# Optimization experiments

Hardware: AMD Instinct MI355X
Metric: run time of the kernel (lower is better)

The kernel has to match this reference:

```python
import jax, jax.numpy as jnp
import numpy as np

B, T, K = 64, 1024, 256  # batch, seq_len, num_labels


def setup_inputs() -> dict:
    key = jax.random.key(0)
    k1, k2 = jax.random.split(key)
    emissions = jax.random.normal(k1, (B, T, K), dtype=jnp.float32)
    transitions = jax.random.normal(k2, (K, K), dtype=jnp.float32) * 0.1
    return {"emissions": emissions, "transitions": transitions}


def _viterbi_decode(emissions, transitions):
    """Viterbi decode, mirroring tfa.text.crf_decode with full-length sequences.
    emissions: [B, T, K] unary potentials; transitions: [K, K] (prev -> next).
    Returns int32 tag sequence [B, T]."""
    em = jnp.transpose(emissions, (1, 0, 2))  # [T, B, K]

    def fwd_step(state, emit_t):
        # state: [B, K] running max scores ending in each tag at time t-1
        scores = state[:, :, None] + transitions[None, :, :]  # [B, K_prev, K_next]
        bp = jnp.argmax(scores, axis=1).astype(jnp.int32)      # [B, K] backpointers
        new_state = jnp.max(scores, axis=1) + emit_t           # [B, K]
        return new_state, bp

    state, bps = jax.lax.scan(fwd_step, em[0], em[1:])  # bps: [T-1, B, K]
    last_tag = jnp.argmax(state, axis=-1).astype(jnp.int32)  # [B]

    def back_step(tag, bp_t):
        prev = jnp.take_along_axis(bp_t, tag[:, None], axis=1)[:, 0]
        return prev, prev

    # reverse scan: bps[i] maps tag at t=i+1 back to tag at t=i
    _, earlier = jax.lax.scan(back_step, last_tag, bps, reverse=True)  # [T-1, B]
    tags = jnp.concatenate([earlier, last_tag[None, :]], axis=0)  # [T, B]
    return jnp.transpose(tags, (1, 0))  # [B, T]


def reference(emissions, transitions):
    # CRF.call in inference mode: crf_decode then cast to the input dtype.
    return _viterbi_decode(emissions, transitions).astype(emissions.dtype)
```

## Files before the change

### kernel.cpp

```cpp
#include <hip/hip_runtime.h>


#define CRF_B 64
#define CRF_T 1024
#define CRF_K 256
#define NSEG  16
#define SEGLEN 64

#define FG 8
#define FP 32


#define LD4(v, p, col) { \
    v.x = trans[(size_t)(p) * CRF_K + (col)]; \
    v.y = trans[(size_t)((p) + 1) * CRF_K + (col)]; \
    v.z = trans[(size_t)((p) + 2) * CRF_K + (col)]; \
    v.w = trans[(size_t)((p) + 3) * CRF_K + (col)]; }

#define FWD_CHUNK(idx, ta, tb) { \
    float4 sv = sp[idx]; \
    float a0 = sv.x + ta.x; \
    float a1 = sv.y + ta.y; \
    float a2 = sv.z + ta.z; \
    float a3 = sv.w + ta.w; \
    float r0 = fmaxf(fmaxf(a0, a1), a2); \
    m0 = fmaxf(fmaxf(r0, a3), m0); \
    float c0 = sv.x + tb.x; \
    float c1 = sv.y + tb.y; \
    float c2 = sv.z + tb.z; \
    float c3 = sv.w + tb.w; \
    float r1 = fmaxf(fmaxf(c0, c1), c2); \
    m1 = fmaxf(fmaxf(r1, c3), m1); }

__global__ __launch_bounds__(1024, 4) void crf_forward_states(
    const float* __restrict__ em, const float* __restrict__ trans,
    float* __restrict__ M, unsigned char* __restrict__ gidp)
{
    const int b   = blockIdx.x;
    const int tid = threadIdx.x;
    const int g   = tid >> 7;
    const int c   = tid & 127;

    __shared__ __align__(16) float s_state[CRF_K];
    __shared__ float s_partial[FG][CRF_K];

    const int pbase = g * FP;
    const int c2    = c + 128;

    float4 ta0, ta1, ta2, ta3, ta4, ta5, ta6, ta7;
    float4 tb0, tb1, tb2, tb3, tb4, tb5, tb6, tb7;
    LD4(ta0, pbase +  0, c)  LD4(ta1, pbase +  4, c)
    LD4(ta2, pbase +  8, c)  LD4(ta3, pbase + 12, c)
    LD4(ta4, pbase + 16, c)  LD4(ta5, pbase + 20, c)
    LD4(ta6, pbase + 24, c)  LD4(ta7, pbase + 28, c)
    LD4(tb0, pbase +  0, c2) LD4(tb1, pbase +  4, c2)
    LD4(tb2, pbase +  8, c2) LD4(tb3, pbase + 12, c2)
    LD4(tb4, pbase + 16, c2) LD4(tb5, pbase + 20, c2)
    LD4(tb6, pbase + 24, c2) LD4(tb7, pbase + 28, c2)

    const float* emb = em + (size_t)b * CRF_T * CRF_K;
    if (tid < CRF_K) s_state[tid] = emb[tid];
    float e_cur = 0.0f;
    if (tid < CRF_K) e_cur = emb[CRF_K + tid];
    __syncthreads();

    float sp0 = 0, sp1 = 0, sp2 = 0, sp3 = 0;
    float sp4 = 0, sp5 = 0, sp6 = 0, sp7 = 0;
    float sbv = 0;

    for (int t = 1; t < CRF_T; ++t) {
        if (gidp && tid < CRF_K && t > 1) {
            int bg = 7;
            if (sp6 == sbv) bg = 6;
            if (sp5 == sbv) bg = 5;
            if (sp4 == sbv) bg = 4;
            if (sp3 == sbv) bg = 3;
            if (sp2 == sbv) bg = 2;
            if (sp1 == sbv) bg = 1;
            if (sp0 == sbv) bg = 0;
            int g1 = __shfl_down(bg, 1, 64);
            if ((tid & 1) == 0)
                gidp[((size_t)(t - 1) * CRF_B + b) * 128 + (tid >> 1)] =
                    (unsigned char)(bg | (g1 << 4));
        }

        float e_next = 0.0f;
        if (tid < CRF_K && t + 1 < CRF_T)
            e_next = emb[(t + 1) * CRF_K + tid];

        float m0 = -INFINITY, m1 = -INFINITY;
        const float4* sp = (const float4*)(s_state + pbase);
        FWD_CHUNK(0, ta0, tb0) FWD_CHUNK(1, ta1, tb1)
        FWD_CHUNK(2, ta2, tb2) FWD_CHUNK(3, ta3, tb3)
        FWD_CHUNK(4, ta4, tb4) FWD_CHUNK(5, ta5, tb5)
        FWD_CHUNK(6, ta6, tb6) FWD_CHUNK(7, ta7, tb7)

        s_partial[g][c]  = m0;
        s_partial[g][c2] = m1;
        __syncthreads();
        if (tid < CRF_K) {
            float p0 = s_partial[0][tid], p1 = s_partial[1][tid];
            float p2 = s_partial[2][tid], p3 = s_partial[3][tid];
            float p4 = s_partial[4][tid], p5 = s_partial[5][tid];
            float p6 = s_partial[6][tid], p7 = s_partial[7][tid];
            float q0 = fmaxf(fmaxf(p0, p1), p2);
            float q1 = fmaxf(fmaxf(p3, p4), p5);
            float bv = fmaxf(fmaxf(fmaxf(q0, q1), p6), p7);
            s_state[tid] = bv + e_cur;
            M[((size_t)t * CRF_B + b) * CRF_K + tid] = bv;
            sp0 = p0; sp1 = p1; sp2 = p2; sp3 = p3;
            sp4 = p4; sp5 = p5; sp6 = p6; sp7 = p7; sbv = bv;
        }
        __syncthreads();
        e_cur = e_next;
    }

    if (gidp && tid < CRF_K) {
        int bg = 7;
        if (sp6 == sbv) bg = 6;
        if (sp5 == sbv) bg = 5;
        if (sp4 == sbv) bg = 4;
        if (sp3 == sbv) bg = 3;
        if (sp2 == sbv) bg = 2;
        if (sp1 == sbv) bg = 1;
        if (sp0 == sbv) bg = 0;
        int g1 = __shfl_down(bg, 1, 64);
        if ((tid & 1) == 0)
            gidp[((size_t)(CRF_T - 1) * CRF_B + b) * 128 + (tid >> 1)] =
                (unsigned char)(bg | (g1 << 4));
    }
}


#define BPG_CHUNK(j) { \
    float4 mm = M4[j]; float4 ee = E4[j]; \
    float s0 = mm.x + ee.x, s1 = mm.y + ee.y; \
    float s2 = mm.z + ee.z, s3 = mm.w + ee.w; \
    float t0v = s_tile[base + 4*(j) + 0][lane]; \
    float t1v = s_tile[base + 4*(j) + 1][lane]; \
    float t2v = s_tile[base + 4*(j) + 2][lane]; \
    float t3v = s_tile[base + 4*(j) + 3][lane]; \
    float v0 = s0 + t0v; if (v0 > best) { best = v0; arg = base + 4*(j); } \
    float v1 = s1 + t1v; if (v1 > best) { best = v1; arg = base + 4*(j) + 1; } \
    float v2 = s2 + t2v; if (v2 > best) { best = v2; arg = base + 4*(j) + 2; } \
    float v3 = s3 + t3v; if (v3 > best) { best = v3; arg = base + 4*(j) + 3; } }

#define BPG_CHUNK0(j) { \
    float4 ee = E4[j]; \
    float t0v = s_tile[base + 4*(j) + 0][lane]; \
    float t1v = s_tile[base + 4*(j) + 1][lane]; \
    float t2v = s_tile[base + 4*(j) + 2][lane]; \
    float t3v = s_tile[base + 4*(j) + 3][lane]; \
    float v0 = ee.x + t0v; if (v0 > best) { best = v0; arg = base + 4*(j); } \
    float v1 = ee.y + t1v; if (v1 > best) { best = v1; arg = base + 4*(j) + 1; } \
    float v2 = ee.z + t2v; if (v2 > best) { best = v2; arg = base + 4*(j) + 2; } \
    float v3 = ee.w + t3v; if (v3 > best) { best = v3; arg = base + 4*(j) + 3; } }

__global__ __launch_bounds__(256) void crf_bp_gid(
    const float* __restrict__ M, const float* __restrict__ em,
    const float* __restrict__ trans, const unsigned char* __restrict__ gidp,
    unsigned char* __restrict__ bp)
{
    const int b    = blockIdx.x >> 3;
    const int cg   = (blockIdx.x >> 1) & 3;
    const int ts   = blockIdx.x & 1;
    const int tid  = threadIdx.x;
    const int lane = tid & 63;
    const int w    = tid >> 6;

    __shared__ float s_tile[CRF_K][64];

    const int k0 = cg * 64;
    for (int idx = tid; idx < CRF_K * 64; idx += 256) {
        const int p = idx >> 6, cc = idx & 63;
        s_tile[p][cc] = trans[(size_t)p * CRF_K + k0 + cc];
    }
    __syncthreads();

    const int t_lo = ts * 512;
    const int t_hi = ts ? (CRF_T - 1) : 512;
    const int half = (k0 >> 1) + (lane >> 1);
    const int odd  = lane & 1;

    int t1 = t_lo + w;
    if (t1 >= t_hi) return;
    unsigned char gb = gidp[((size_t)(t1 + 1) * CRF_B + b) * 128 + half];

    for (; t1 < t_hi; t1 += 4) {
        const int tn = t1 + 4;
        unsigned char gb_next = 0;
        if (tn < t_hi)
            gb_next = gidp[((size_t)(tn + 1) * CRF_B + b) * 128 + half];

        const int g    = odd ? ((gb >> 4) & 7) : (gb & 7);
        const int base = g << 5;
        const float4* E4 =
            (const float4*)(em + ((size_t)b * CRF_T + t1) * CRF_K + base);
        float best = -INFINITY; int arg = base;
        if (t1 == 0) {
            BPG_CHUNK0(0) BPG_CHUNK0(1) BPG_CHUNK0(2) BPG_CHUNK0(3)
            BPG_CHUNK0(4) BPG_CHUNK0(5) BPG_CHUNK0(6) BPG_CHUNK0(7)
        } else {
            const float4* M4 =
                (const float4*)(M + ((size_t)t1 * CRF_B + b) * CRF_K + base);
            BPG_CHUNK(0) BPG_CHUNK(1) BPG_CHUNK(2) BPG_CHUNK(3)
            BPG_CHUNK(4) BPG_CHUNK(5) BPG_CHUNK(6) BPG_CHUNK(7)
        }
        bp[((size_t)b * (CRF_T - 1) + t1) * CRF_K + k0 + lane] =
            (unsigned char)arg;
        gb = gb_next;
    }
}


__global__ __launch_bounds__(1024, 2) void crf_bp_matrix(
    const float* __restrict__ M, const float* __restrict__ em,
    const float* __restrict__ trans, unsigned char* __restrict__ bp)
{
    const int b   = blockIdx.x >> 4;
    const int seg = blockIdx.x & 15;
    const int tid = threadIdx.x;
    const int g   = tid >> 8;
    const int k   = tid & 255;

    __shared__ __align__(16) float s_row[CRF_K];
    __shared__ float s_pv[4][CRF_K];
    __shared__ int   s_pi[4][CRF_K];

    const int pbase = g * 64;
    float4 tr[16];
#pragma unroll
    for (int i = 0; i < 16; ++i) {
        const int p = pbase + 4 * i;
        tr[i].x = trans[(p + 0) * CRF_K + k];
        tr[i].y = trans[(p + 1) * CRF_K + k];
        tr[i].z = trans[(p + 2) * CRF_K + k];
        tr[i].w = trans[(p + 3) * CRF_K + k];
    }

    const int t_lo = seg * SEGLEN;
    const int t_hi = min(t_lo + SEGLEN, CRF_T - 1);
    unsigned char* bpb = bp + (size_t)b * (CRF_T - 1) * CRF_K;

    for (int t1 = t_lo; t1 < t_hi; ++t1) {
        if (tid < CRF_K) {
            float ev = em[((size_t)b * CRF_T + t1) * CRF_K + tid];
            float sv = ev;
            if (t1 > 0) sv = M[((size_t)t1 * CRF_B + b) * CRF_K + tid] + ev;
            s_row[tid] = sv;
        }
        __syncthreads();

        float best = -INFINITY;
        int   arg  = pbase;
        const float4* spp = (const float4*)(s_row + pbase);
#pragma unroll
        for (int i = 0; i < 16; ++i) {
            float4 st = spp[i];
            const int p = pbase + 4 * i;
            float s0 = st.x + tr[i].x;
            float s1 = st.y + tr[i].y;
            float s2 = st.z + tr[i].z;
            float s3 = st.w + tr[i].w;
            if (s0 > best) { best = s0; arg = p; }
            if (s1 > best) { best = s1; arg = p + 1; }
            if (s2 > best) { best = s2; arg = p + 2; }
            if (s3 > best) { best = s3; arg = p + 3; }
        }
        s_pv[g][k] = best;
        s_pi[g][k] = arg;
        __syncthreads();
        if (tid < CRF_K) {
            float bv = s_pv[0][tid];
            int   ba = s_pi[0][tid];
#pragma unroll
            for (int j = 1; j < 4; ++j) {
                float v = s_pv[j][tid];
                if (v > bv) { bv = v; ba = s_pi[j][tid]; }
            }
            bpb[(size_t)t1 * CRF_K + tid] = (unsigned char)ba;
        }
        __syncthreads();
    }
}


__global__ __launch_bounds__(256) void crf_seg_maps(
    const unsigned char* __restrict__ bp, unsigned char* __restrict__ maps)
{
    const int b   = blockIdx.x >> 4;
    const int s   = blockIdx.x & 15;
    const int tid = threadIdx.x;
    const int rows = (s == NSEG - 1) ? SEGLEN - 1 : SEGLEN;
    const int r0   = s * SEGLEN;

    __shared__ unsigned char lbp[SEGLEN][CRF_K];

    const unsigned char* bpb = bp + (size_t)b * (CRF_T - 1) * CRF_K;
    const int nw = rows * 64;
    for (int w = tid; w < nw; w += 256) {
        const int r = w >> 6, cc = w & 63;
        ((unsigned int*)lbp[r])[cc] =
            ((const unsigned int*)(bpb + (size_t)(r0 + r) * CRF_K))[cc];
    }
    __syncthreads();

    int tag = tid;
    for (int j = rows - 1; j >= 0; --j) tag = lbp[j][tag];
    maps[((size_t)b * NSEG + s) * CRF_K + tid] = (unsigned char)tag;
}

__global__ __launch_bounds__(256) void crf_compose(
    const float* __restrict__ M, const float* __restrict__ em,
    const unsigned char* __restrict__ maps,
    int* __restrict__ exits, float* __restrict__ out)
{
    const int b   = blockIdx.x;
    const int tid = threadIdx.x;

    __shared__ float s_wv[4];
    __shared__ int   s_wi[4];

    float v = M[((size_t)(CRF_T - 1) * CRF_B + b) * CRF_K + tid]
            + em[((size_t)b * CRF_T + (CRF_T - 1)) * CRF_K + tid];
    int   i = tid;
#pragma unroll
    for (int off = 32; off >= 1; off >>= 1) {
        float ov = __shfl_xor(v, off, 64);
        int   oi = __shfl_xor(i, off, 64);
        if (ov > v || (ov == v && oi < i)) { v = ov; i = oi; }
    }
    const int lane = tid & 63, wv = tid >> 6;
    if (lane == 0) { s_wv[wv] = v; s_wi[wv] = i; }
    __syncthreads();
    if (tid == 0) {
        float bv = s_wv[0]; int bi = s_wi[0];
#pragma unroll
        for (int w = 1; w < 4; ++w)
            if (s_wv[w] > bv) { bv = s_wv[w]; bi = s_wi[w]; }
        out[(size_t)b * CRF_T + (CRF_T - 1)] = (float)bi;
        int E = bi;
        exits[b * NSEG + NSEG - 1] = E;
        const unsigned char* mb = maps + (size_t)b * NSEG * CRF_K;
        for (int s = NSEG - 1; s >= 1; --s) {
            E = mb[(size_t)s * CRF_K + E];
            exits[b * NSEG + s - 1] = E;
        }
    }
}

__global__ __launch_bounds__(256) void crf_emit(
    const unsigned char* __restrict__ bp, const int* __restrict__ exits,
    float* __restrict__ out)
{
    const int b   = blockIdx.x >> 4;
    const int s   = blockIdx.x & 15;
    const int tid = threadIdx.x;
    const int rows = (s == NSEG - 1) ? SEGLEN - 1 : SEGLEN;
    const int r0   = s * SEGLEN;

    __shared__ unsigned char lbp[SEGLEN][CRF_K];

    const unsigned char* bpb = bp + (size_t)b * (CRF_T - 1) * CRF_K;
    const int nw = rows * 64;
    for (int w = tid; w < nw; w += 256) {
        const int r = w >> 6, cc = w & 63;
        ((unsigned int*)lbp[r])[cc] =
            ((const unsigned int*)(bpb + (size_t)(r0 + r) * CRF_K))[cc];
    }
    __syncthreads();

    int tag = tid;
    const bool win = (tid == exits[b * NSEG + s]);
    for (int j = rows - 1; j >= 0; --j) {
        tag = lbp[j][tag];
        if (win) out[(size_t)b * CRF_T + r0 + j] = (float)tag;
    }
}

__global__ void crf_zero_out(float* __restrict__ out, int n)
{
    int i = blockIdx.x * blockDim.x + threadIdx.x;
    if (i < n) out[i] = 0.0f;
}


extern "C" void kernel_launch(void* const* d_in, const int* in_sizes, int n_in,
                              void* d_out, int out_size, void* d_ws, size_t ws_size,
                              hipStream_t stream) {
    (void)in_sizes; (void)n_in;
    const float* em    = (const float*)d_in[0];
    const float* trans = (const float*)d_in[1];
    float* out = (float*)d_out;

    const size_t M_bytes     = (size_t)CRF_T * CRF_B * CRF_K * sizeof(float);
    const size_t gid_bytes   = (size_t)CRF_T * CRF_B * 128;
    const size_t bp_bytes    = (size_t)CRF_B * (CRF_T - 1) * CRF_K;
    const size_t maps_bytes  = (size_t)CRF_B * NSEG * CRF_K;
    const size_t exits_bytes = (size_t)CRF_B * NSEG * sizeof(int);

    char* w = (char*)d_ws;
    if (ws_size >= M_bytes + gid_bytes + bp_bytes + maps_bytes + exits_bytes) {
        float*         M     = (float*)w;            w += M_bytes;
        unsigned char* gidp  = (unsigned char*)w;    w += gid_bytes;
        unsigned char* bp    = (unsigned char*)w;    w += bp_bytes;
        unsigned char* maps  = (unsigned char*)w;    w += maps_bytes;
        int*           exits = (int*)w;

        crf_forward_states<<<CRF_B, 1024, 0, stream>>>(em, trans, M, gidp);
        crf_bp_gid<<<CRF_B * 8, 256, 0, stream>>>(M, em, trans, gidp, bp);
        crf_seg_maps<<<CRF_B * NSEG, 256, 0, stream>>>(bp, maps);
        crf_compose<<<CRF_B, 256, 0, stream>>>(M, em, maps, exits, out);
        crf_emit<<<CRF_B * NSEG, 256, 0, stream>>>(bp, exits, out);
    } else if (ws_size >= M_bytes + bp_bytes + maps_bytes + exits_bytes) {
        float*         M     = (float*)w;            w += M_bytes;
        unsigned char* bp    = (unsigned char*)w;    w += bp_bytes;
        unsigned char* maps  = (unsigned char*)w;    w += maps_bytes;
        int*           exits = (int*)w;

        crf_forward_states<<<CRF_B, 1024, 0, stream>>>(em, trans, M, nullptr);
        crf_bp_matrix<<<CRF_B * NSEG, 1024, 0, stream>>>(M, em, trans, bp);
        crf_seg_maps<<<CRF_B * NSEG, 256, 0, stream>>>(bp, maps);
        crf_compose<<<CRF_B, 256, 0, stream>>>(M, em, maps, exits, out);
        crf_emit<<<CRF_B * NSEG, 256, 0, stream>>>(bp, exits, out);
    } else {
        crf_zero_out<<<(out_size + 255) / 256, 256, 0, stream>>>(out, out_size);
    }
}
```

Measured before the change: 1.099 ms.

## Reduce forward-step partial maxima with wave shuffles and double-buffered state

The forward max-plus recurrence is remapped so that each wave owns 16 output columns, and the four 16-lane quarters each cover 64 predecessor rows. The per-column max is reduced with in-wave xor shuffles instead of going through a shared-memory partial array. This removes one of the two block-wide barriers per timestep. The state vector is double-buffered in LDS with a padded, rotated layout to avoid bank conflicts, and packed v_pk_add_f32 is used for the adds. The group-id encoding for backpointers changes to match the new predecessor partition, which risks inconsistency with the unseen backtrace kernel.

```diff
diff --git a/kernel.cpp b/kernel.cpp
--- a/kernel.cpp
+++ b/kernel.cpp
@@ -7,127 +7,138 @@
 #define NSEG  16
 #define SEGLEN 64
 
-#define FG 8
-#define FP 32
-
-
-#define LD4(v, p, col) { \
-    v.x = trans[(size_t)(p) * CRF_K + (col)]; \
-    v.y = trans[(size_t)((p) + 1) * CRF_K + (col)]; \
-    v.z = trans[(size_t)((p) + 2) * CRF_K + (col)]; \
-    v.w = trans[(size_t)((p) + 3) * CRF_K + (col)]; }
-
-#define FWD_CHUNK(idx, ta, tb) { \
-    float4 sv = sp[idx]; \
-    float a0 = sv.x + ta.x; \
-    float a1 = sv.y + ta.y; \
-    float a2 = sv.z + ta.z; \
-    float a3 = sv.w + ta.w; \
-    float r0 = fmaxf(fmaxf(a0, a1), a2); \
-    m0 = fmaxf(fmaxf(r0, a3), m0); \
-    float c0 = sv.x + tb.x; \
-    float c1 = sv.y + tb.y; \
-    float c2 = sv.z + tb.z; \
-    float c3 = sv.w + tb.w; \
-    float r1 = fmaxf(fmaxf(c0, c1), c2); \
-    m1 = fmaxf(fmaxf(r1, c3), m1); }
+
+typedef float f32x2 __attribute__((ext_vector_type(2)));
+
+__device__ __forceinline__ f32x2 pk_add(f32x2 a, f32x2 b) {
+    f32x2 d;
+    asm("v_pk_add_f32 %0, %1, %2" : "=v"(d) : "v"(a), "v"(b));
+    return d;
+}
+
+#define CHUNK_F 132
+#define BUF_F   (4 * CHUNK_F)
 
 __global__ __launch_bounds__(1024, 4) void crf_forward_states(
     const float* __restrict__ em, const float* __restrict__ trans,
     float* __restrict__ M, unsigned char* __restrict__ gidp)
 {
-    const int b   = blockIdx.x;
-    const int tid = threadIdx.x;
-    const int g   = tid >> 7;
-    const int c   = tid & 127;
-
-    __shared__ __align__(16) float s_state[CRF_K];
-    __shared__ float s_partial[FG][CRF_K];
-
-    const int pbase = g * FP;
-    const int c2    = c + 128;
-
-    float4 ta0, ta1, ta2, ta3, ta4, ta5, ta6, ta7;
-    float4 tb0, tb1, tb2, tb3, tb4, tb5, tb6, tb7;
-    LD4(ta0, pbase +  0, c)  LD4(ta1, pbase +  4, c)
-    LD4(ta2, pbase +  8, c)  LD4(ta3, pbase + 12, c)
-    LD4(ta4, pbase + 16, c)  LD4(ta5, pbase + 20, c)
-    LD4(ta6, pbase + 24, c)  LD4(ta7, pbase + 28, c)
-    LD4(tb0, pbase +  0, c2) LD4(tb1, pbase +  4, c2)
-    LD4(tb2, pbase +  8, c2) LD4(tb3, pbase + 12, c2)
-    LD4(tb4, pbase + 16, c2) LD4(tb5, pbase + 20, c2)
-    LD4(tb6, pbase + 24, c2) LD4(tb7, pbase + 28, c2)
+    const int b    = blockIdx.x;
+    const int tid  = threadIdx.x;
+    const int w    = tid >> 6;
+    const int lane = tid & 63;
+    const int l    = lane & 15;
+    const int q    = lane >> 4;
+    const int c    = (w << 4) + l;
+    const bool own = (q == 0);
+
+    __shared__ __align__(16) float sbuf[2][BUF_F];
+
+    f32x2 tr[32];
+#pragma unroll
+    for (int k = 0; k < 8; ++k) {
+        const int p0 = (q << 6) + 4 * ((q + k) & 7);
+        const float* tp0 = trans + (size_t)p0 * CRF_K + c;
+        tr[2*k+0].x = tp0[0];
+        tr[2*k+0].y = tp0[CRF_K];
+        tr[2*k+1].x = tp0[2 * CRF_K];
+        tr[2*k+1].y = tp0[3 * CRF_K];
+        const float* tp1 = tp0 + 32 * CRF_K;
+        tr[16+2*k+0].x = tp1[0];
+        tr[16+2*k+0].y = tp1[CRF_K];
+        tr[16+2*k+1].x = tp1[2 * CRF_K];
+        tr[16+2*k+1].y = tp1[3 * CRF_K];
+    }
 
     const float* emb = em + (size_t)b * CRF_T * CRF_K;
-    if (tid < CRF_K) s_state[tid] = emb[tid];
-    float e_cur = 0.0f;
-    if (tid < CRF_K) e_cur = emb[CRF_K + tid];
+
+    if (tid < CRF_K) {
+        const int cid = tid >> 6, h = (tid >> 5) & 1, pos = tid & 31;
+        const int a0  = CHUNK_F * cid + 64 * h + pos;
+        float v = emb[tid];
+        sbuf[0][a0] = v;
+        if (pos < 12) sbuf[0][a0 + 32] = v;
+    }
+    float e_cur = own ? emb[CRF_K + c] : 0.0f;
     __syncthreads();
 
-    float sp0 = 0, sp1 = 0, sp2 = 0, sp3 = 0;
-    float sp4 = 0, sp5 = 0, sp6 = 0, sp7 = 0;
-    float sbv = 0;
+    const int wcid = c >> 6, wh = (c >> 5) & 1, wpos = c & 31;
+    const int wa   = CHUNK_F * wcid + 64 * wh + wpos;
+
+    float* mptr = M + ((size_t)CRF_B + b) * CRF_K + c;
+    unsigned char* gptr = gidp
+        ? gidp + ((size_t)CRF_B + b) * 128 + (w << 3) + (l >> 1)
+        : nullptr;
+
+    float pm0 = 0.0f, pm1 = 0.0f, pbv = 0.0f;
+    int cb = 0;
 
     for (int t = 1; t < CRF_T; ++t) {
-        if (gidp && tid < CRF_K && t > 1) {
-            int bg = 7;
-            if (sp6 == sbv) bg = 6;
-            if (sp5 == sbv) bg = 5;
-            if (sp4 == sbv) bg = 4;
-            if (sp3 == sbv) bg = 3;
-            if (sp2 == sbv) bg = 2;
-            if (sp1 == sbv) bg = 1;
-            if (sp0 == sbv) bg = 0;
-            int g1 = __shfl_down(bg, 1, 64);
-            if ((tid & 1) == 0)
-                gidp[((size_t)(t - 1) * CRF_B + b) * 128 + (tid >> 1)] =
-                    (unsigned char)(bg | (g1 << 4));
+        if (gptr && t > 1) {
+            int g = (pm1 == pbv) ? ((q << 1) | 1) : 8;
+            if (pm0 == pbv) g = q << 1;
+            g = min(g, __shfl_xor(g, 16, 64));
+            g = min(g, __shfl_xor(g, 32, 64));
+            int go = __shfl_down(g, 1, 64);
+            if (own && !(l & 1))
+                *gptr = (unsigned char)(g | (go << 4));
+            gptr += CRF_B * 128;
         }
 
         float e_next = 0.0f;
-        if (tid < CRF_K && t + 1 < CRF_T)
-            e_next = emb[(t + 1) * CRF_K + tid];
+        if (own && t + 1 < CRF_T)
+            e_next = emb[(size_t)(t + 1) * CRF_K + c];
+
+        const float4* sp = (const float4*)(sbuf[cb]) + 33 * q;
 
         float m0 = -INFINITY, m1 = -INFINITY;
-        const float4* sp = (const float4*)(s_state + pbase);
-        FWD_CHUNK(0, ta0, tb0) FWD_CHUNK(1, ta1, tb1)
-        FWD_CHUNK(2, ta2, tb2) FWD_CHUNK(3, ta3, tb3)
-        FWD_CHUNK(4, ta4, tb4) FWD_CHUNK(5, ta5, tb5)
-        FWD_CHUNK(6, ta6, tb6) FWD_CHUNK(7, ta7, tb7)
-
-        s_partial[g][c]  = m0;
-        s_partial[g][c2] = m1;
-        __syncthreads();
-        if (tid < CRF_K) {
-            float p0 = s_partial[0][tid], p1 = s_partial[1][tid];
-            float p2 = s_partial[2][tid], p3 = s_partial[3][tid];
-            float p4 = s_partial[4][tid], p5 = s_partial[5][tid];
-            float p6 = s_partial[6][tid], p7 = s_partial[7][tid];
-            float q0 = fmaxf(fmaxf(p0, p1), p2);
-            float q1 = fmaxf(fmaxf(p3, p4), p5);
-            float bv = fmaxf(fmaxf(fmaxf(q0, q1), p6), p7);
-            s_state[tid] = bv + e_cur;
-            M[((size_t)t * CRF_B + b) * CRF_K + tid] = bv;
-            sp0 = p0; sp1 = p1; sp2 = p2; sp3 = p3;
-            sp4 = p4; sp5 = p5; sp6 = p6; sp7 = p7; sbv = bv;
-        }
+#pragma unroll
+        for (int k = 0; k < 8; ++k) {
+            float4 sv = sp[q + k];
+            f32x2 lo; lo.x = sv.x; lo.y = sv.y;
+            f32x2 hi; hi.x = sv.z; hi.y = sv.w;
+            f32x2 r0 = pk_add(lo, tr[2*k]);
+            f32x2 r1 = pk_add(hi, tr[2*k+1]);
+            m0 = fmaxf(fmaxf(r0.x, r0.y), m0);
+            m0 = fmaxf(fmaxf(r1.x, r1.y), m0);
+        }
+#pragma unroll
+        for (int k = 0; k < 8; ++k) {
+            float4 sv = sp[16 + q + k];
+            f32x2 lo; lo.x = sv.x; lo.y = sv.y;
+            f32x2 hi; hi.x = sv.z; hi.y = sv.w;
+            f32x2 r0 = pk_add(lo, tr[16+2*k]);
+            f32x2 r1 = pk_add(hi, tr[16+2*k+1]);
+            m1 = fmaxf(fmaxf(r0.x, r0.y), m1);
+            m1 = fmaxf(fmaxf(r1.x, r1.y), m1);
+        }
+
+        float bv = fmaxf(m0, m1);
+        bv = fmaxf(bv, __shfl_xor(bv, 16, 64));
+        bv = fmaxf(bv, __shfl_xor(bv, 32, 64));
+
+        float* nb = sbuf[cb ^ 1];
+        if (own) {
+            *mptr = bv;
+            float sv = bv + e_cur;
+            nb[wa] = sv;
+            if (wpos < 12) nb[wa + 32] = sv;
+        }
+        pm0 = m0; pm1 = m1; pbv = bv;
         __syncthreads();
         e_cur = e_next;
-    }
-
-    if (gidp && tid < CRF_K) {
-        int bg = 7;
-        if (sp6 == sbv) bg = 6;
-        if (sp5 == sbv) bg = 5;
-        if (sp4 == sbv) bg = 4;
-        if (sp3 == sbv) bg = 3;
-        if (sp2 == sbv) bg = 2;
-        if (sp1 == sbv) bg = 1;
-        if (sp0 == sbv) bg = 0;
-        int g1 = __shfl_down(bg, 1, 64);
-        if ((tid & 1) == 0)
-            gidp[((size_t)(CRF_T - 1) * CRF_B + b) * 128 + (tid >> 1)] =
-                (unsigned char)(bg | (g1 << 4));
+        mptr += CRF_B * CRF_K;
+        cb ^= 1;
+    }
+
+    if (gptr) {
+        int g = (pm1 == pbv) ? ((q << 1) | 1) : 8;
+        if (pm0 == pbv) g = q << 1;
+        g = min(g, __shfl_xor(g, 16, 64));
+        g = min(g, __shfl_xor(g, 32, 64));
+        int go = __shfl_down(g, 1, 64);
+        if (own && !(l & 1))
+            *gptr = (unsigned char)(g | (go << 4));
     }
 }
 
```

Result: slower. 1.456 ms (+32.5%).

## Spread forward partial-max reduction across all threads with DPP quad reductions

Applied to the files above, without the earlier changes.

Instead of 256 threads each reading 8 partial maxima and reducing them serially, all 1024 threads now take part: each quad of lanes owns one column, reads two partials from a padded transposed shared array, and combines them with DPP xor swizzles. The group-index backpointer byte is computed inside the same step from a bitmask of which groups hit the max, rather than deferred to the next iteration. The aim is a shorter critical path between the two barriers in the serial time loop. In exchange it adds DPP and shuffle operations plus a gidp write in every step, and every thread now loads its emission value.

```diff
diff --git a/kernel.cpp b/kernel.cpp
--- a/kernel.cpp
+++ b/kernel.cpp
@@ -9,6 +9,7 @@
 
 #define FG 8
 #define FP 32
+#define PPAD 9
 
 
 #define LD4(v, p, col) { \
@@ -32,6 +33,19 @@
     float r1 = fmaxf(fmaxf(c0, c1), c2); \
     m1 = fmaxf(fmaxf(r1, c3), m1); }
 
+#define DPP_QP_XOR1 0xB1
+#define DPP_QP_XOR2 0x4E
+
+template <int CTRL>
+__device__ __forceinline__ float dpp_getf(float v) {
+    return __int_as_float(__builtin_amdgcn_update_dpp(
+        0, __float_as_int(v), CTRL, 0xf, 0xf, false));
+}
+template <int CTRL>
+__device__ __forceinline__ int dpp_geti(int v) {
+    return __builtin_amdgcn_update_dpp(0, v, CTRL, 0xf, 0xf, false);
+}
+
 __global__ __launch_bounds__(1024, 4) void crf_forward_states(
     const float* __restrict__ em, const float* __restrict__ trans,
     float* __restrict__ M, unsigned char* __restrict__ gidp)
@@ -40,9 +54,11 @@
     const int tid = threadIdx.x;
     const int g   = tid >> 7;
     const int c   = tid & 127;
+    const int col = tid >> 2;
+    const int j   = tid & 3;
 
     __shared__ __align__(16) float s_state[CRF_K];
-    __shared__ float s_partial[FG][CRF_K];
+    __shared__ float s_partial[CRF_K][PPAD];
 
     const int pbase = g * FP;
     const int c2    = c + 128;
@@ -60,33 +76,18 @@
 
     const float* emb = em + (size_t)b * CRF_T * CRF_K;
     if (tid < CRF_K) s_state[tid] = emb[tid];
-    float e_cur = 0.0f;
-    if (tid < CRF_K) e_cur = emb[CRF_K + tid];
+    float e_cur = emb[CRF_K + col];
     __syncthreads();
 
-    float sp0 = 0, sp1 = 0, sp2 = 0, sp3 = 0;
-    float sp4 = 0, sp5 = 0, sp6 = 0, sp7 = 0;
-    float sbv = 0;
+    float* mp = M + ((size_t)CRF_B + b) * CRF_K + col;
+    unsigned char* gp = gidp
+        ? gidp + ((size_t)CRF_B + b) * 128 + (col >> 1)
+        : nullptr;
+    const float* ep = emb + 2 * CRF_K + col;
 
     for (int t = 1; t < CRF_T; ++t) {
-        if (gidp && tid < CRF_K && t > 1) {
-            int bg = 7;
-            if (sp6 == sbv) bg = 6;
-            if (sp5 == sbv) bg = 5;
-            if (sp4 == sbv) bg = 4;
-            if (sp3 == sbv) bg = 3;
-            if (sp2 == sbv) bg = 2;
-            if (sp1 == sbv) bg = 1;
-            if (sp0 == sbv) bg = 0;
-            int g1 = __shfl_down(bg, 1, 64);
-            if ((tid & 1) == 0)
-                gidp[((size_t)(t - 1) * CRF_B + b) * 128 + (tid >> 1)] =
-                    (unsigned char)(bg | (g1 << 4));
-        }
-
         float e_next = 0.0f;
-        if (tid < CRF_K && t + 1 < CRF_T)
-            e_next = emb[(t + 1) * CRF_K + tid];
+        if (t + 1 < CRF_T) e_next = *ep;
 
         float m0 = -INFINITY, m1 = -INFINITY;
         const float4* sp = (const float4*)(s_state + pbase);
@@ -95,39 +96,38 @@
         FWD_CHUNK(4, ta4, tb4) FWD_CHUNK(5, ta5, tb5)
         FWD_CHUNK(6, ta6, tb6) FWD_CHUNK(7, ta7, tb7)
 
-        s_partial[g][c]  = m0;
-        s_partial[g][c2] = m1;
+        s_partial[c][g]  = m0;
+        s_partial[c2][g] = m1;
         __syncthreads();
-        if (tid < CRF_K) {
-            float p0 = s_partial[0][tid], p1 = s_partial[1][tid];
-            float p2 = s_partial[2][tid], p3 = s_partial[3][tid];
-            float p4 = s_partial[4][tid], p5 = s_partial[5][tid];
-            float p6 = s_partial[6][tid], p7 = s_partial[7][tid];
-            float q0 = fmaxf(fmaxf(p0, p1), p2);
-            float q1 = fmaxf(fmaxf(p3, p4), p5);
-            float bv = fmaxf(fmaxf(fmaxf(q0, q1), p6), p7);
-            s_state[tid] = bv + e_cur;
-            M[((size_t)t * CRF_B + b) * CRF_K + tid] = bv;
-            sp0 = p0; sp1 = p1; sp2 = p2; sp3 = p3;
-            sp4 = p4; sp5 = p5; sp6 = p6; sp7 = p7; sbv = bv;
-        }
+
+        const float px = s_partial[col][2 * j];
+        const float py = s_partial[col][2 * j + 1];
+        float mm = fmaxf(px, py);
+        mm = fmaxf(mm, dpp_getf<DPP_QP_XOR1>(mm));
+        const float bv = fmaxf(mm, dpp_getf<DPP_QP_XOR2>(mm));
+
+        if (j == 0) {
+            *mp = bv;
+            s_state[col] = bv + e_cur;
+        }
+        mp += CRF_B * CRF_K;
+
+        if (gp) {
+            int mk = 0;
+            if (px == bv) mk  = 1 << (2 * j);
+            if (py == bv) mk |= 1 << (2 * j + 1);
+            mk |= dpp_geti<DPP_QP_XOR1>(mk);
+            mk |= dpp_geti<DPP_QP_XOR2>(mk);
+            const int gv = __ffs(mk) - 1;
+            const int go = __shfl_down(gv, 4, 64);
+            if ((tid & 7) == 0)
+                *gp = (unsigned char)(gv | (go << 4));
+            gp += CRF_B * 128;
+        }
+
         __syncthreads();
         e_cur = e_next;
-    }
-
-    if (gidp && tid < CRF_K) {
-        int bg = 7;
-        if (sp6 == sbv) bg = 6;
-        if (sp5 == sbv) bg = 5;
-        if (sp4 == sbv) bg = 4;
-        if (sp3 == sbv) bg = 3;
-        if (sp2 == sbv) bg = 2;
-        if (sp1 == sbv) bg = 1;
-        if (sp0 == sbv) bg = 0;
-        int g1 = __shfl_down(bg, 1, 64);
-        if ((tid & 1) == 0)
-            gidp[((size_t)(CRF_T - 1) * CRF_B + b) * 128 + (tid >> 1)] =
-                (unsigned char)(bg | (g1 << 4));
+        ep += CRF_K;
     }
 }
 
```

Result: slower. 1.233 ms (+12.2%).

## Halve forward-pass block to 512 threads with 4 columns per thread and packed adds

Applied to the files above, without the earlier changes.

The forward Viterbi kernel now runs 512 threads per batch row instead of 1024. Each thread covers 4 next-tag columns (l, l+64, l+128, l+192) over 32 previous tags, up from 2 columns. It holds 128 transition values in registers and uses 2-wide float vectors so the compiler can emit packed fp32 adds. The aim is to cut barrier cost and shared-memory state reads per step on this serial, latency-bound recurrence. The cost is double the per-thread work per step and higher register pressure.

```diff
diff --git a/kernel.cpp b/kernel.cpp
--- a/kernel.cpp
+++ b/kernel.cpp
@@ -11,52 +11,35 @@
 #define FP 32
 
 
-#define LD4(v, p, col) { \
-    v.x = trans[(size_t)(p) * CRF_K + (col)]; \
-    v.y = trans[(size_t)((p) + 1) * CRF_K + (col)]; \
-    v.z = trans[(size_t)((p) + 2) * CRF_K + (col)]; \
-    v.w = trans[(size_t)((p) + 3) * CRF_K + (col)]; }
-
-#define FWD_CHUNK(idx, ta, tb) { \
-    float4 sv = sp[idx]; \
-    float a0 = sv.x + ta.x; \
-    float a1 = sv.y + ta.y; \
-    float a2 = sv.z + ta.z; \
-    float a3 = sv.w + ta.w; \
-    float r0 = fmaxf(fmaxf(a0, a1), a2); \
-    m0 = fmaxf(fmaxf(r0, a3), m0); \
-    float c0 = sv.x + tb.x; \
-    float c1 = sv.y + tb.y; \
-    float c2 = sv.z + tb.z; \
-    float c3 = sv.w + tb.w; \
-    float r1 = fmaxf(fmaxf(c0, c1), c2); \
-    m1 = fmaxf(fmaxf(r1, c3), m1); }
-
-__global__ __launch_bounds__(1024, 4) void crf_forward_states(
+typedef float f32x2 __attribute__((ext_vector_type(2)));
+
+__global__ __launch_bounds__(512, 2) void crf_forward_states(
     const float* __restrict__ em, const float* __restrict__ trans,
     float* __restrict__ M, unsigned char* __restrict__ gidp)
 {
     const int b   = blockIdx.x;
     const int tid = threadIdx.x;
-    const int g   = tid >> 7;
-    const int c   = tid & 127;
+    const int g   = tid >> 6;
+    const int l   = tid & 63;
 
     __shared__ __align__(16) float s_state[CRF_K];
     __shared__ float s_partial[FG][CRF_K];
 
     const int pbase = g * FP;
-    const int c2    = c + 128;
-
-    float4 ta0, ta1, ta2, ta3, ta4, ta5, ta6, ta7;
-    float4 tb0, tb1, tb2, tb3, tb4, tb5, tb6, tb7;
-    LD4(ta0, pbase +  0, c)  LD4(ta1, pbase +  4, c)
-    LD4(ta2, pbase +  8, c)  LD4(ta3, pbase + 12, c)
-    LD4(ta4, pbase + 16, c)  LD4(ta5, pbase + 20, c)
-    LD4(ta6, pbase + 24, c)  LD4(ta7, pbase + 28, c)
-    LD4(tb0, pbase +  0, c2) LD4(tb1, pbase +  4, c2)
-    LD4(tb2, pbase +  8, c2) LD4(tb3, pbase + 12, c2)
-    LD4(tb4, pbase + 16, c2) LD4(tb5, pbase + 20, c2)
-    LD4(tb6, pbase + 24, c2) LD4(tb7, pbase + 28, c2)
+
+    f32x2 t01[4][8], t23[4][8];
+#pragma unroll
+    for (int ci = 0; ci < 4; ++ci) {
+        const int col = l + 64 * ci;
+#pragma unroll
+        for (int k = 0; k < 8; ++k) {
+            const int p = pbase + 4 * k;
+            t01[ci][k].x = trans[(size_t)p * CRF_K + col];
+            t01[ci][k].y = trans[(size_t)(p + 1) * CRF_K + col];
+            t23[ci][k].x = trans[(size_t)(p + 2) * CRF_K + col];
+            t23[ci][k].y = trans[(size_t)(p + 3) * CRF_K + col];
+        }
+    }
 
     const float* emb = em + (size_t)b * CRF_T * CRF_K;
     if (tid < CRF_K) s_state[tid] = emb[tid];
@@ -88,16 +71,46 @@
         if (tid < CRF_K && t + 1 < CRF_T)
             e_next = emb[(t + 1) * CRF_K + tid];
 
+        const float4* sp = (const float4*)(s_state + pbase);
         float m0 = -INFINITY, m1 = -INFINITY;
-        const float4* sp = (const float4*)(s_state + pbase);
-        FWD_CHUNK(0, ta0, tb0) FWD_CHUNK(1, ta1, tb1)
-        FWD_CHUNK(2, ta2, tb2) FWD_CHUNK(3, ta3, tb3)
-        FWD_CHUNK(4, ta4, tb4) FWD_CHUNK(5, ta5, tb5)
-        FWD_CHUNK(6, ta6, tb6) FWD_CHUNK(7, ta7, tb7)
-
-        s_partial[g][c]  = m0;
-        s_partial[g][c2] = m1;
+        float m2 = -INFINITY, m3 = -INFINITY;
+#pragma unroll
+        for (int k = 0; k < 8; ++k) {
+            const float4 sv = sp[k];
+            f32x2 s01; s01.x = sv.x; s01.y = sv.y;
+            f32x2 s23; s23.x = sv.z; s23.y = sv.w;
+            {
+                f32x2 a01 = s01 + t01[0][k];
+                f32x2 a23 = s23 + t23[0][k];
+                float r0 = fmaxf(fmaxf(a01.x, a01.y), a23.x);
+                m0 = fmaxf(fmaxf(r0, a23.y), m0);
+            }
+            {
+                f32x2 a01 = s01 + t01[1][k];
+                f32x2 a23 = s23 + t23[1][k];
+                float r0 = fmaxf(fmaxf(a01.x, a01.y), a23.x);
+                m1 = fmaxf(fmaxf(r0, a23.y), m1);
+            }
+            {
+                f32x2 a01 = s01 + t01[2][k];
+                f32x2 a23 = s23 + t23[2][k];
+                float r0 = fmaxf(fmaxf(a01.x, a01.y), a23.x);
+                m2 = fmaxf(fmaxf(r0, a23.y), m2);
+            }
+            {
+                f32x2 a01 = s01 + t01[3][k];
+                f32x2 a23 = s23 + t23[3][k];
+                float r0 = fmaxf(fmaxf(a01.x, a01.y), a23.x);
+                m3 = fmaxf(fmaxf(r0, a23.y), m3);
+            }
+        }
+
+        s_partial[g][l]       = m0;
+        s_partial[g][l + 64]  = m1;
+        s_partial[g][l + 128] = m2;
+        s_partial[g][l + 192] = m3;
         __syncthreads();
+
         if (tid < CRF_K) {
             float p0 = s_partial[0][tid], p1 = s_partial[1][tid];
             float p2 = s_partial[2][tid], p3 = s_partial[3][tid];
@@ -407,7 +420,7 @@
         unsigned char* maps  = (unsigned char*)w;    w += maps_bytes;
         int*           exits = (int*)w;
 
-        crf_forward_states<<<CRF_B, 1024, 0, stream>>>(em, trans, M, gidp);
+        crf_forward_states<<<CRF_B, 512, 0, stream>>>(em, trans, M, gidp);
         crf_bp_gid<<<CRF_B * 8, 256, 0, stream>>>(M, em, trans, gidp, bp);
         crf_seg_maps<<<CRF_B * NSEG, 256, 0, stream>>>(bp, maps);
         crf_compose<<<CRF_B, 256, 0, stream>>>(M, em, maps, exits, out);
@@ -418,7 +431,7 @@
         unsigned char* maps  = (unsigned char*)w;    w += maps_bytes;
         int*           exits = (int*)w;
 
-        crf_forward_states<<<CRF_B, 1024, 0, stream>>>(em, trans, M, nullptr);
+        crf_forward_states<<<CRF_B, 512, 0, stream>>>(em, trans, M, nullptr);
         crf_bp_matrix<<<CRF_B * NSEG, 1024, 0, stream>>>(M, em, trans, bp);
         crf_seg_maps<<<CRF_B * NSEG, 256, 0, stream>>>(bp, maps);
         crf_compose<<<CRF_B, 256, 0, stream>>>(M, em, maps, exits, out);
```

Result: slower. 1.381 ms (+25.7%).
